# Optimization experiments

Hardware: AMD Instinct MI355X
Metric: run time of the kernel (lower is better)

Reference implementation:

```python
import jax, jax.numpy as jnp
import numpy as np
import math

INPUT_WIDTH = 1024
KEY_WIDTH = 64
VALUE_WIDTH = 64
NUM_HEADS = 16
NUM_GROUPS = 4
HEADS_PER_GROUP = NUM_HEADS // NUM_GROUPS  # w = 4


def setup_inputs() -> dict:
    key = jax.random.key(0)
    k_x, k_q, k_k, k_v, k_p = jax.random.split(key, 5)
    n, s = 2, 2048
    # torch.nn.Linear weights are [out, in]; we store transposed [in, out] for x @ W.
    def lin(k, fan_in, fan_out):
        bound = 1.0 / math.sqrt(fan_in)
        return jax.random.uniform(k, (fan_in, fan_out), minval=-bound, maxval=bound, dtype=jnp.float32)
    return {
        "X": jax.random.normal(k_x, (n, s, INPUT_WIDTH), dtype=jnp.float32),
        "Wq": lin(k_q, INPUT_WIDTH, NUM_HEADS * KEY_WIDTH),
        "Wk": lin(k_k, INPUT_WIDTH, NUM_GROUPS * KEY_WIDTH),
        "Wv": lin(k_v, INPUT_WIDTH, NUM_GROUPS * VALUE_WIDTH),
        "Wpost": lin(k_p, NUM_HEADS * VALUE_WIDTH, INPUT_WIDTH),
    }


def reference(X, Wq, Wk, Wv, Wpost):
    n, s, _ = X.shape
    # Projections (no bias)
    Q = (X @ Wq).reshape(n, s, NUM_GROUPS, HEADS_PER_GROUP, KEY_WIDTH)  # [b,s,g,w,e]
    K = (X @ Wk).reshape(n, s, NUM_GROUPS, KEY_WIDTH)                   # [b,t,g,e]
    V = (X @ Wv).reshape(n, s, NUM_GROUPS, VALUE_WIDTH)                 # [b,t,g,e]
    scale = 1.0 / math.sqrt(KEY_WIDTH)
    # Grouped cross-attention: scores [b,s,t,g,w]
    raw = jnp.einsum('bsgwe,btge->bstgw', Q, K * scale)
    attn = jax.nn.softmax(raw, axis=2)  # softmax over key positions t
    A = jnp.einsum('bstgw,btge->bsgwe', attn, V).reshape(n, s, NUM_HEADS * VALUE_WIDTH)
    P = A @ Wpost
    return X + P
```

## Files before the change

kernel.cpp:

```cpp
#include <hip/hip_runtime.h>
#include <hip/hip_bf16.h>
#include <hip/hip_fp16.h>
#include <math.h>

typedef __attribute__((ext_vector_type(8))) short bfrag8;
typedef __attribute__((ext_vector_type(8))) _Float16 hfrag8;
typedef __attribute__((ext_vector_type(4))) float facc4;
typedef __attribute__((ext_vector_type(16))) float facc16;

#define MFMA16B(a, b, c) __builtin_amdgcn_mfma_f32_16x16x32_bf16((a), (b), (c), 0, 0, 0)
#define MFMA32B(a, b, c) __builtin_amdgcn_mfma_f32_32x32x16_bf16((a), (b), (c), 0, 0, 0)
#define MFMA32H(a, b, c) __builtin_amdgcn_mfma_f32_32x32x16_f16((a), (b), (c), 0, 0, 0)

__device__ __forceinline__ void gload_lds16(const void* g, void* l) {
    __builtin_amdgcn_global_load_lds(
        (const __attribute__((address_space(1))) void*)g,
        (__attribute__((address_space(3))) void*)l, 16, 0, 0);
}

__device__ __forceinline__ unsigned short f2bf(float f) {
    unsigned u = __float_as_uint(f);
    u += 0x7fffu + ((u >> 16) & 1u);
    return (unsigned short)(u >> 16);
}

__device__ __forceinline__ unsigned pk2(float a, float b) {
    auto h = __builtin_amdgcn_cvt_pkrtz(a, b);
    union { decltype(h) h; unsigned u; } c;
    c.h = h;
    return c.u;
}

__device__ __forceinline__ void do_transpose(const float* __restrict__ src,
                                             unsigned short* __restrict__ dst,
                                             int Kdim, int N, int nb, int kb,
                                             float (*tile)[33], int tid) {
    int tx = tid & 31, ty = tid >> 5;
#pragma unroll
    for (int r = ty; r < 32; r += 8)
        tile[r][tx] = src[(size_t)(kb + r) * N + nb + tx];
    __syncthreads();
#pragma unroll
    for (int r = ty; r < 32; r += 8)
        dst[(size_t)(nb + r) * Kdim + kb + tx] = f2bf(tile[tx][r]);
}

__global__ __launch_bounds__(256) void k_prep(
    const float* __restrict__ X, const float* __restrict__ Wq,
    const float* __restrict__ Wk, const float* __restrict__ Wv,
    const float* __restrict__ Wp,
    unsigned short* __restrict__ Xb, unsigned short* __restrict__ Wqkvt,
    unsigned short* __restrict__ Wpt) {
    __shared__ float tile[32][33];
    int blk = blockIdx.x, tid = threadIdx.x;
    if (blk < 4096) {
        int i = (blk * 256 + tid) * 4;
        float4 v = *reinterpret_cast<const float4*>(X + i);
        unsigned short o[4] = {f2bf(v.x), f2bf(v.y), f2bf(v.z), f2bf(v.w)};
        *reinterpret_cast<ulonglong1*>(Xb + i) = *reinterpret_cast<ulonglong1*>(o);
    } else if (blk < 5120) {
        int idx = blk - 4096;
        do_transpose(Wq, Wqkvt, 1024, 1024, (idx & 31) * 32, (idx >> 5) * 32, tile, tid);
    } else if (blk < 5376) {
        int idx = blk - 5120;
        do_transpose(Wk, Wqkvt + 1024 * 1024, 1024, 256, (idx & 7) * 32, (idx >> 3) * 32, tile, tid);
    } else if (blk < 5632) {
        int idx = blk - 5376;
        do_transpose(Wv, Wqkvt + 1280 * 1024, 1024, 256, (idx & 7) * 32, (idx >> 3) * 32, tile, tid);
    } else {
        int idx = blk - 5632;
        do_transpose(Wp, Wpt, 1024, 1024, (idx & 31) * 32, (idx >> 5) * 32, tile, tid);
    }
}

template <int EPI>
__global__ __launch_bounds__(512) void k_gemm_bt(
    const unsigned short* __restrict__ A, const unsigned short* __restrict__ Bt,
    int M, int N, int K,
    unsigned short* __restrict__ Qo, unsigned short* __restrict__ Ko,
    unsigned short* __restrict__ Vto,
    const float* __restrict__ Xres, float* __restrict__ Out) {
    __shared__ char lds[49152];
    const int tid = threadIdx.x;
    const int lane = tid & 63, wid = tid >> 6;
    const int wr = wid >> 1, wc = wid & 1;
    const int l15 = lane & 15, lhi = lane >> 4;
    const int m0 = blockIdx.y * 128, n0 = blockIdx.x * 64;
    const int nk = K >> 6;

    facc4 acc[2][2] = {};

    auto STAGE = [&](int buf, int k0) {
#pragma unroll
        for (int i = 0; i < 2; ++i) {
            int p = (wid * 2 + i) * 1024 + lane * 16;
            int row = p >> 7;
            int src = (p & 127) ^ ((row & 7) << 4);
            gload_lds16(A + (size_t)(m0 + row) * K + k0 + (src >> 1),
                        lds + buf * 16384 + (wid * 2 + i) * 1024);
        }
        {
            int p = wid * 1024 + lane * 16;
            int row = p >> 7;
            int src = (p & 127) ^ ((row & 7) << 4);
            gload_lds16(Bt + (size_t)(n0 + row) * K + k0 + (src >> 1),
                        lds + 32768 + buf * 8192 + wid * 1024);
        }
    };

    STAGE(0, 0);
    __syncthreads();

    for (int t = 0; t < nk; ++t) {
        const int cur = t & 1;
        if (t + 1 < nk) STAGE(cur ^ 1, (t + 1) * 64);
        const char* Ab = lds + cur * 16384;
        const char* Bb = lds + 32768 + cur * 8192;
#pragma unroll
        for (int kc = 0; kc < 2; ++kc) {
            bfrag8 af[2], bfv[2];
#pragma unroll
            for (int mi = 0; mi < 2; ++mi) {
                int row = wr * 32 + mi * 16 + l15;
                int off = (row * 128 + kc * 64 + lhi * 16) ^ ((row & 7) << 4);
                af[mi] = *reinterpret_cast<const bfrag8*>(Ab + off);
            }
#pragma unroll
            for (int ni = 0; ni < 2; ++ni) {
                int row = wc * 32 + ni * 16 + l15;
                int off = (row * 128 + kc * 64 + lhi * 16) ^ ((row & 7) << 4);
                bfv[ni] = *reinterpret_cast<const bfrag8*>(Bb + off);
            }
#pragma unroll
            for (int mi = 0; mi < 2; ++mi)
#pragma unroll
                for (int ni = 0; ni < 2; ++ni)
                    acc[mi][ni] = MFMA16B(af[mi], bfv[ni], acc[mi][ni]);
        }
        __syncthreads();
    }

    if (EPI == 0 && n0 >= 1280) {
        unsigned short* VT = (unsigned short*)lds;
#pragma unroll
        for (int mi = 0; mi < 2; ++mi)
#pragma unroll
            for (int ni = 0; ni < 2; ++ni) {
                int col = wc * 32 + ni * 16 + l15;
                int row0 = wr * 32 + mi * 16 + lhi * 4;
                unsigned long long u = 0;
#pragma unroll
                for (int r = 0; r < 4; ++r)
                    u |= (unsigned long long)__half_as_ushort(__float2half(acc[mi][ni][r]))
                         << (16 * r);
                *reinterpret_cast<unsigned long long*>(VT + col * 136 + row0) = u;
            }
        __syncthreads();
        int c = tid >> 3, part = tid & 7;
        int b = m0 >> 11;
        int g = (n0 - 1280) >> 6;
        unsigned short* dstp =
            Vto + ((size_t)(b * 4 + g) * 64 + c) * 2048 + (m0 & 2047) + part * 16;
        const unsigned short* srcp = VT + c * 136 + part * 16;
        *(reinterpret_cast<uint4*>(dstp) + 0) = *(reinterpret_cast<const uint4*>(srcp) + 0);
        *(reinterpret_cast<uint4*>(dstp) + 1) = *(reinterpret_cast<const uint4*>(srcp) + 1);
        return;
    }

#pragma unroll
    for (int mi = 0; mi < 2; ++mi)
#pragma unroll
        for (int ni = 0; ni < 2; ++ni)
#pragma unroll
            for (int r = 0; r < 4; ++r) {
                int grow = m0 + wr * 32 + mi * 16 + lhi * 4 + r;
                int gcol = n0 + wc * 32 + ni * 16 + l15;
                float v = acc[mi][ni][r];
                if (EPI == 0) {
                    int b = grow >> 11, t = grow & 2047;
                    if (gcol < 1024) {
                        Qo[(size_t)grow * 1024 + gcol] = f2bf(v * 0.18033688f);
                    } else {
                        int cc = gcol - 1024;
                        int g = cc >> 6, e = cc & 63;
                        Ko[(((size_t)(b * 4 + g) * 2048 + t) << 6) + e] = f2bf(v);
                    }
                } else {
                    size_t idx = (size_t)grow * 1024 + gcol;
                    Out[idx] = Xres[idx] + v;
                }
            }
}

__global__ __launch_bounds__(512, 2) void k_attn(
    const unsigned short* __restrict__ Q,
    const unsigned short* __restrict__ Kb,
    const unsigned short* __restrict__ Vt,
    unsigned short* __restrict__ Abuf) {
    __shared__ char smem[49152];

    const int tid = threadIdx.x;
    const int lane = tid & 63, wid = tid >> 6;
    const int kvh = wid >> 2, qw = wid & 3;
    const int l31 = lane & 31, hi = lane >> 5;

    int wg = blockIdx.x;
    int swz = ((wg & 7) << 6) | (wg >> 3);
    const int qt = swz & 15, head = (swz >> 4) & 15, b = swz >> 8;
    const int g = head >> 2;
    const size_t kvK = (size_t)(b * 4 + g) * 2048 * 64;
    const size_t kvV = (size_t)(b * 4 + g) * 64 * 2048;
    const int qrow0 = b * 2048 + qt * 128 + qw * 32;

    bfrag8 qf[4];
#pragma unroll
    for (int ks = 0; ks < 4; ++ks)
        qf[ks] = *reinterpret_cast<const bfrag8*>(
            Q + (size_t)(qrow0 + l31) * 1024 + head * 64 + ks * 16 + hi * 8);

    const int p = qw * 1024 + lane * 16;
    const int rK = p >> 7;
    const int cK = (p & 127) ^ ((rK & 7) << 4);
    const unsigned short* srcK = Kb + kvK + (size_t)(kvh * 1024 + rK) * 64 + (cK >> 1);
    const int rV = p >> 6;
    const int cV = (p & 63) ^ ((rV & 6) << 3);
    const unsigned short* srcV = Vt + kvV + (size_t)rV * 2048 + kvh * 1024 + (cV >> 1);
    const int dK = kvh * 12288 + qw * 1024;
    const int dV = 24576 + kvh * 12288 + qw * 1024;

    facc16 o[2] = {};
    float psA = 0.f, psB = 0.f;

    gload_lds16(srcK, smem + dK);
    gload_lds16(srcV, smem + dV);
    gload_lds16(srcK + 32 * 64, smem + dK + 4096);
    gload_lds16(srcV + 32, smem + dV + 4096);

    for (int t = 0; t < 32; ++t) {
        if (t < 31) asm volatile("s_waitcnt vmcnt(2)" ::: "memory");
        else        asm volatile("s_waitcnt vmcnt(0)" ::: "memory");
        __builtin_amdgcn_s_barrier();
        __builtin_amdgcn_sched_barrier(0);
        if (t < 30) {
            const int bn = (t + 2) % 3;
            gload_lds16(srcK + (size_t)(t + 2) * (32 * 64), smem + dK + bn * 4096);
            gload_lds16(srcV + (size_t)(t + 2) * 32, smem + dV + bn * 4096);
        }
        const char* Kc = smem + kvh * 12288 + (t % 3) * 4096;
        const char* Vc = smem + 24576 + kvh * 12288 + (t % 3) * 4096;

        facc16 s = {};
        __builtin_amdgcn_s_setprio(1);
#pragma unroll
        for (int ks = 0; ks < 4; ++ks) {
            int off = (l31 * 128 + ks * 32 + hi * 16) ^ ((l31 & 7) << 4);
            bfrag8 kf = *reinterpret_cast<const bfrag8*>(Kc + off);
            s = MFMA32B(kf, qf[ks], s);
        }
        __builtin_amdgcn_s_setprio(0);

#pragma unroll
        for (int e = 0; e < 16; e += 2) {
            float e0 = __builtin_amdgcn_exp2f(s[e]);
            float e1 = __builtin_amdgcn_exp2f(s[e + 1]);
            s[e] = e0;
            s[e + 1] = e1;
            psA += e0;
            psB += e1;
        }
#pragma unroll
        for (int kh = 0; kh < 2; ++kh) {
            const int pb = kh * 2;
            unsigned a0 = pk2(s[4 * pb + 0], s[4 * pb + 1]);
            unsigned a1 = pk2(s[4 * pb + 2], s[4 * pb + 3]);
            unsigned b0 = pk2(s[4 * pb + 4], s[4 * pb + 5]);
            unsigned b1 = pk2(s[4 * pb + 6], s[4 * pb + 7]);
            asm("v_permlane32_swap_b32 %0, %1" : "+v"(a0), "+v"(b0));
            asm("v_permlane32_swap_b32 %0, %1" : "+v"(a1), "+v"(b1));
            union { unsigned u[4]; hfrag8 h; } pu;
            pu.u[0] = a0; pu.u[1] = a1; pu.u[2] = b0; pu.u[3] = b1;
            __builtin_amdgcn_s_setprio(1);
#pragma unroll
            for (int ot = 0; ot < 2; ++ot) {
                int row = ot * 32 + l31;
                int off = row * 64 + ((kh * 32 + hi * 16) ^ ((row & 6) << 3));
                hfrag8 vf = *reinterpret_cast<const hfrag8*>(Vc + off);
                o[ot] = MFMA32H(vf, pu.h, o[ot]);
            }
            __builtin_amdgcn_s_setprio(0);
        }
    }
    __syncthreads();

    float psum = psA + psB;
    float* cmO = (float*)smem;
    float* cmL = (float*)(smem + 32768);
    if (kvh == 1) {
#pragma unroll
        for (int ot = 0; ot < 2; ++ot)
#pragma unroll
            for (int r = 0; r < 16; ++r)
                cmO[qw * 2048 + (ot * 16 + r) * 64 + lane] = o[ot][r];
        cmL[qw * 64 + lane] = psum;
    }
    __syncthreads();
    if (kvh == 0) {
#pragma unroll
        for (int ot = 0; ot < 2; ++ot)
#pragma unroll
            for (int r = 0; r < 16; ++r)
                o[ot][r] += cmO[qw * 2048 + (ot * 16 + r) * 64 + lane];
        psum += cmL[qw * 64 + lane];

        float l = psum + __shfl_xor(psum, 32, 64);
        float rl = 1.0f / l;
        int arow = qrow0 + l31;
#pragma unroll
        for (int ot = 0; ot < 2; ++ot)
#pragma unroll
            for (int p2 = 0; p2 < 4; ++p2) {
                unsigned long long u = 0;
#pragma unroll
                for (int r = 0; r < 4; ++r)
                    u |= (unsigned long long)f2bf(o[ot][4 * p2 + r] * rl) << (16 * r);
                *reinterpret_cast<unsigned long long*>(
                    Abuf + (size_t)arow * 1024 + head * 64 + ot * 32 + p2 * 8 + hi * 4) = u;
            }
    }
}


extern "C" void kernel_launch(void* const* d_in, const int* in_sizes, int n_in,
                              void* d_out, int out_size, void* d_ws, size_t ws_size,
                              hipStream_t stream) {
    const float* X = (const float*)d_in[0];
    const float* Wq = (const float*)d_in[1];
    const float* Wk = (const float*)d_in[2];
    const float* Wv = (const float*)d_in[3];
    const float* Wpost = (const float*)d_in[4];
    float* Out = (float*)d_out;

    unsigned short* Xb = (unsigned short*)d_ws;
    unsigned short* Wqkvt = Xb + 4096 * 1024;
    unsigned short* Wpt = Wqkvt + 1536 * 1024;
    unsigned short* Qb = Wpt + 1024 * 1024;
    unsigned short* Kbuf = Qb + 4096 * 1024;
    unsigned short* Vtbuf = Kbuf + 8 * 2048 * 64;
    unsigned short* Abuf = Vtbuf + 8 * 2048 * 64;

    k_prep<<<6656, 256, 0, stream>>>(X, Wq, Wk, Wv, Wpost, Xb, Wqkvt, Wpt);

    k_gemm_bt<0><<<dim3(24, 32), 512, 0, stream>>>(Xb, Wqkvt, 4096, 1536, 1024,
                                                   Qb, Kbuf, Vtbuf, nullptr, nullptr);

    k_attn<<<512, 512, 0, stream>>>(Qb, Kbuf, Vtbuf, Abuf);

    k_gemm_bt<1><<<dim3(16, 32), 512, 0, stream>>>(Abuf, Wpt, 4096, 1024, 1024,
                                                   nullptr, nullptr, nullptr, X, Out);
}
```

Before: 89.43 us.

## Split attention KV range across four wave groups with double-buffered LDS

Doubles the attention block to 1024 threads so four wave groups each handle a quarter of the key/value sequence (16 tiles instead of 32), then reduces the partial outputs and sums through LDS in two passes. The pipeline drops from a triple buffer with vmcnt waits to a double buffer with a full __syncthreads every iteration. The aim is more parallelism per query tile to shorten the serial loop. In exchange it uses more LDS (64KB), adds a larger cross-wave reduction, and syncs a 16-wave block every tile. With launch_bounds(1024,2) the register budget per thread is also tighter.

```diff
diff --git a/kernel.cpp b/kernel.cpp
--- a/kernel.cpp
+++ b/kernel.cpp
@@ -192,12 +192,12 @@
             }
 }
 
-__global__ __launch_bounds__(512, 2) void k_attn(
+__global__ __launch_bounds__(1024, 2) void k_attn(
     const unsigned short* __restrict__ Q,
     const unsigned short* __restrict__ Kb,
     const unsigned short* __restrict__ Vt,
     unsigned short* __restrict__ Abuf) {
-    __shared__ char smem[49152];
+    __shared__ char smem[65536];
 
     const int tid = threadIdx.x;
     const int lane = tid & 63, wid = tid >> 6;
@@ -221,41 +221,37 @@
     const int p = qw * 1024 + lane * 16;
     const int rK = p >> 7;
     const int cK = (p & 127) ^ ((rK & 7) << 4);
-    const unsigned short* srcK = Kb + kvK + (size_t)(kvh * 1024 + rK) * 64 + (cK >> 1);
+    const unsigned short* srcK = Kb + kvK + (size_t)(kvh * 512 + rK) * 64 + (cK >> 1);
     const int rV = p >> 6;
     const int cV = (p & 63) ^ ((rV & 6) << 3);
-    const unsigned short* srcV = Vt + kvV + (size_t)rV * 2048 + kvh * 1024 + (cV >> 1);
-    const int dK = kvh * 12288 + qw * 1024;
-    const int dV = 24576 + kvh * 12288 + qw * 1024;
+    const unsigned short* srcV = Vt + kvV + (size_t)rV * 2048 + kvh * 512 + (cV >> 1);
+    const int dK = kvh * 8192 + qw * 1024;
+    const int dV = 32768 + kvh * 8192 + qw * 1024;
 
     facc16 o[2] = {};
+    const facc16 fz = {};
     float psA = 0.f, psB = 0.f;
 
     gload_lds16(srcK, smem + dK);
     gload_lds16(srcV, smem + dV);
-    gload_lds16(srcK + 32 * 64, smem + dK + 4096);
-    gload_lds16(srcV + 32, smem + dV + 4096);
-
-    for (int t = 0; t < 32; ++t) {
-        if (t < 31) asm volatile("s_waitcnt vmcnt(2)" ::: "memory");
-        else        asm volatile("s_waitcnt vmcnt(0)" ::: "memory");
-        __builtin_amdgcn_s_barrier();
-        __builtin_amdgcn_sched_barrier(0);
-        if (t < 30) {
-            const int bn = (t + 2) % 3;
-            gload_lds16(srcK + (size_t)(t + 2) * (32 * 64), smem + dK + bn * 4096);
-            gload_lds16(srcV + (size_t)(t + 2) * 32, smem + dV + bn * 4096);
-        }
-        const char* Kc = smem + kvh * 12288 + (t % 3) * 4096;
-        const char* Vc = smem + 24576 + kvh * 12288 + (t % 3) * 4096;
-
-        facc16 s = {};
+    __syncthreads();
+
+    for (int t = 0; t < 16; ++t) {
+        const int cur = t & 1;
+        if (t < 15) {
+            gload_lds16(srcK + (size_t)(t + 1) * (32 * 64), smem + dK + (cur ^ 1) * 4096);
+            gload_lds16(srcV + (size_t)(t + 1) * 32, smem + dV + (cur ^ 1) * 4096);
+        }
+        const char* Kc = smem + kvh * 8192 + cur * 4096;
+        const char* Vc = smem + 32768 + kvh * 8192 + cur * 4096;
+
+        facc16 s;
         __builtin_amdgcn_s_setprio(1);
 #pragma unroll
         for (int ks = 0; ks < 4; ++ks) {
             int off = (l31 * 128 + ks * 32 + hi * 16) ^ ((l31 & 7) << 4);
             bfrag8 kf = *reinterpret_cast<const bfrag8*>(Kc + off);
-            s = MFMA32B(kf, qf[ks], s);
+            s = MFMA32B(kf, qf[ks], ks == 0 ? fz : s);
         }
         __builtin_amdgcn_s_setprio(0);
 
@@ -289,29 +285,35 @@
             }
             __builtin_amdgcn_s_setprio(0);
         }
-    }
-    __syncthreads();
+        __syncthreads();
+    }
 
     float psum = psA + psB;
-    float* cmO = (float*)smem;
-    float* cmL = (float*)(smem + 32768);
-    if (kvh == 1) {
-#pragma unroll
-        for (int ot = 0; ot < 2; ++ot)
+    float* cm = (float*)smem;
+    float* cmL = (float*)(smem + 49152);
+    const int pb12 = (qw * 3 + kvh - 1);
+#pragma unroll
+    for (int ot = 0; ot < 2; ++ot) {
+        __syncthreads();
+        if (kvh) {
 #pragma unroll
             for (int r = 0; r < 16; ++r)
-                cmO[qw * 2048 + (ot * 16 + r) * 64 + lane] = o[ot][r];
-        cmL[qw * 64 + lane] = psum;
-    }
-    __syncthreads();
+                cm[pb12 * 1024 + r * 64 + lane] = o[ot][r];
+            if (ot == 0) cmL[pb12 * 64 + lane] = psum;
+        }
+        __syncthreads();
+        if (kvh == 0) {
+#pragma unroll
+            for (int j = 0; j < 3; ++j) {
+                const int bb = (qw * 3 + j) * 1024;
+#pragma unroll
+                for (int r = 0; r < 16; ++r)
+                    o[ot][r] += cm[bb + r * 64 + lane];
+                if (ot == 0) psum += cmL[(qw * 3 + j) * 64 + lane];
+            }
+        }
+    }
     if (kvh == 0) {
-#pragma unroll
-        for (int ot = 0; ot < 2; ++ot)
-#pragma unroll
-            for (int r = 0; r < 16; ++r)
-                o[ot][r] += cmO[qw * 2048 + (ot * 16 + r) * 64 + lane];
-        psum += cmL[qw * 64 + lane];
-
         float l = psum + __shfl_xor(psum, 32, 64);
         float rl = 1.0f / l;
         int arow = qrow0 + l31;
@@ -353,7 +355,7 @@
     k_gemm_bt<0><<<dim3(24, 32), 512, 0, stream>>>(Xb, Wqkvt, 4096, 1536, 1024,
                                                    Qb, Kbuf, Vtbuf, nullptr, nullptr);
 
-    k_attn<<<512, 512, 0, stream>>>(Qb, Kbuf, Vtbuf, Abuf);
+    k_attn<<<512, 1024, 0, stream>>>(Qb, Kbuf, Vtbuf, Abuf);
 
     k_gemm_bt<1><<<dim3(16, 32), 512, 0, stream>>>(Abuf, Wpt, 4096, 1024, 1024,
                                                    nullptr, nullptr, nullptr, X, Out);
```

After: 92.93 us. 3.9% more time.
